# Kernel tuning notes

Hardware: AMD Instinct MI355X
Metric: run time of the kernel (lower is better)

## Reference

```python
import math
import jax, jax.numpy as jnp
import numpy as np

B, E, T, C, D, H, FF, L, NC = 16, 25, 300, 3, 64, 8, 256, 4, 60
HD = D // H
EPS = 1e-5


def _ln(x, g, b):
    mu = x.mean(-1, keepdims=True)
    var = ((x - mu) ** 2).mean(-1, keepdims=True)
    return (x - mu) * jax.lax.rsqrt(var + EPS) * g + b


def _pos_encoding(seq_len, d):
    pos = jnp.arange(seq_len, dtype=jnp.float32)[:, None]
    div = jnp.exp(jnp.arange(0, d, 2, dtype=jnp.float32) * (-math.log(10000.0) / d))
    pe = jnp.zeros((seq_len, d), dtype=jnp.float32)
    pe = pe.at[:, 0::2].set(jnp.sin(pos * div))
    pe = pe.at[:, 1::2].set(jnp.cos(pos * div))
    return pe


def setup_inputs() -> dict:
    key = jax.random.key(0)
    ks = jax.random.split(key, 16)
    tn = lambda k, shape: jax.random.truncated_normal(k, -2.0, 2.0, shape, jnp.float32) * 0.02
    inp = {
        "x": jax.random.normal(ks[0], (B, C, T, E), jnp.float32),
        "embed_w": tn(ks[1], (D, C)), "embed_b": jnp.zeros((D,)),
        "eln_g": jnp.ones((D,)), "eln_b": jnp.zeros((D,)),
        "cls": tn(ks[2], (D,)),
        "qkv_w": tn(ks[3], (L, 3 * D, D)), "qkv_b": jnp.zeros((L, 3 * D)),
        "out_w": tn(ks[4], (L, D, D)), "out_b": jnp.zeros((L, D)),
        "ln1_g": jnp.ones((L, D)), "ln1_b": jnp.zeros((L, D)),
        "ln2_g": jnp.ones((L, D)), "ln2_b": jnp.zeros((L, D)),
        "ff1_w": tn(ks[5], (L, FF, D)), "ff1_b": jnp.zeros((L, FF)),
        "ff2_w": tn(ks[6], (L, D, FF)), "ff2_b": jnp.zeros((L, D)),
        "norm_g": jnp.ones((D,)), "norm_b": jnp.zeros((D,)),
        "h1_w": tn(ks[7], (D, D)), "h1_b": jnp.zeros((D,)),
        "h2_w": tn(ks[8], (NC, D)), "h2_b": jnp.zeros((NC,)),
    }
    return inp


def reference(x, embed_w, embed_b, eln_g, eln_b, cls, qkv_w, qkv_b, out_w, out_b,
              ln1_g, ln1_b, ln2_g, ln2_b, ff1_w, ff1_b, ff2_w, ff2_b,
              norm_g, norm_b, h1_w, h1_b, h2_w, h2_b):
    N, S = B * E, T + 1
    # [B,C,T,E] -> [(B E), T, C]
    h = jnp.transpose(x, (0, 3, 2, 1)).reshape(N, T, C)
    h = _ln(h @ embed_w.T + embed_b, eln_g, eln_b)              # embed + LayerNorm
    h = jnp.concatenate([jnp.broadcast_to(cls, (N, 1, D)), h], axis=1)  # prepend cls
    h = h + _pos_encoding(S, D)
    scale = 1.0 / math.sqrt(HD)
    for l in range(L):  # pre-LN torch TransformerEncoderLayer
        y = _ln(h, ln1_g[l], ln1_b[l])
        qkv = y @ qkv_w[l].T + qkv_b[l]                          # [N,S,3D]
        q, k, v = jnp.split(qkv, 3, axis=-1)
        q = q.reshape(N, S, H, HD).transpose(0, 2, 1, 3)
        k = k.reshape(N, S, H, HD).transpose(0, 2, 1, 3)
        v = v.reshape(N, S, H, HD).transpose(0, 2, 1, 3)
        att = jax.nn.softmax(jnp.einsum("nhqd,nhkd->nhqk", q, k) * scale, axis=-1)
        o = jnp.einsum("nhqk,nhkd->nhqd", att, v).transpose(0, 2, 1, 3).reshape(N, S, D)
        h = h + (o @ out_w[l].T + out_b[l])
        y = _ln(h, ln2_g[l], ln2_b[l])
        h = h + (jax.nn.gelu(y @ ff1_w[l].T + ff1_b[l], approximate=False) @ ff2_w[l].T + ff2_b[l])
    feat = h[:, 0].reshape(B, E, D).mean(axis=1)                 # cls pool, mean over edges
    feat = _ln(feat, norm_g, norm_b)
    feat = jax.nn.gelu(feat @ h1_w.T + h1_b, approximate=False)
    return feat @ h2_w.T + h2_b                                  # [B, num_class]
```

## Files before the change

kernel.cpp:

```cpp
#include <hip/hip_runtime.h>
#include <hip/hip_bf16.h>
#include <math.h>

typedef __hip_bfloat16 bf16;
typedef unsigned short u16;
typedef __attribute__((ext_vector_type(8))) short s8b;
typedef __attribute__((ext_vector_type(4))) short s4h;
typedef __attribute__((ext_vector_type(4))) float f32x4;

#define B_N    16
#define E_N    25
#define T_N    300
#define C_N    3
#define D_N    64
#define H_N    8
#define HD_N   8
#define FF_N   256
#define L_N    4
#define NC_N   60
#define N_SEQ  400
#define S_LEN  301
#define NS_TOT 120400
#define NTILES 7525
#define EPS_F  1e-5f
#define N_IN   24
#define CONV_TOT 568576

#define MFMA16(a, b, c) __builtin_amdgcn_mfma_f32_16x16x32_bf16(a, b, c, 0, 0, 0)

struct ConvArgs { const void* src[N_IN]; };

__device__ __forceinline__ float waveSum(float v) {
#pragma unroll
    for (int off = 32; off > 0; off >>= 1) v += __shfl_xor(v, off, 64);
    return v;
}

__device__ __forceinline__ float gelu_exact(float x) {
    return 0.5f * x * (1.0f + erff(x * 0.70710678118654752f));
}

__device__ __forceinline__ u16 f2b(float x) {
    union { bf16 b; u16 s; } u;
    u.b = __float2bfloat16(x);
    return u.s;
}

__device__ __forceinline__ void split1(float x, short* hi, short* lo) {
    union { bf16 b; short s; } uh, ul;
    uh.b = __float2bfloat16(x);
    ul.b = __float2bfloat16(x - __bfloat162float(uh.b));
    *hi = uh.s; *lo = ul.s;
}

__global__ void convert_kernel(ConvArgs args, float* __restrict__ dst) {
    const int sizes[N_IN] = {360000,192,64,64,64,64,49152,768,16384,256,256,256,
                             256,256,65536,1024,65536,256,64,64,4096,64,3840,60};
    const int offs[N_IN]  = {0,360000,360192,360256,360320,360384,360448,409600,
                             410368,426752,427008,427264,427520,427776,428032,
                             493568,494592,560128,560384,560448,560512,564608,
                             564672,568512};
    int t = blockIdx.x;
    int n = sizes[t];
    bool isbf = (((const unsigned short*)args.src[3])[0] == 0x3F80u);
    float* d = dst + offs[t];
    int start  = threadIdx.x + blockIdx.y * blockDim.x;
    int stride = blockDim.x * gridDim.y;
    if (isbf) {
        const unsigned short* s = (const unsigned short*)args.src[t];
        for (int i = start; i < n; i += stride)
            d[i] = __uint_as_float(((unsigned int)s[i]) << 16);
    } else {
        const float* s = (const float*)args.src[t];
        for (int i = start; i < n; i += stride)
            d[i] = s[i];
    }
}

__global__ void split_kernel(const float* __restrict__ src,
                             short* __restrict__ hi, short* __restrict__ lo,
                             int n) {
    int i = blockIdx.x * 256 + threadIdx.x;
    if (i < n) split1(src[i], &hi[i], &lo[i]);
}

__global__ void embed_kernel(const float* __restrict__ x,
                             const float* __restrict__ ew,
                             const float* __restrict__ ebias,
                             const float* __restrict__ g,
                             const float* __restrict__ bb,
                             const float* __restrict__ cls,
                             float* __restrict__ h) {
    int wave = threadIdx.x >> 6;
    int lane = threadIdx.x & 63;
    int row  = blockIdx.x * 4 + wave;
    if (row >= NS_TOT) return;
    int n = row / S_LEN;
    int s = row - n * S_LEN;
    int d = lane;

    float i2  = (float)(d & ~1);
    float div = expf(i2 * (-0.14391156515f));
    float ang = (float)s * div;
    float pe  = (d & 1) ? cosf(ang) : sinf(ang);

    float val;
    if (s == 0) {
        val = cls[d];
    } else {
        int t = s - 1;
        int bidx = n / E_N;
        int e    = n - bidx * E_N;
        int xb   = ((bidx * C_N + 0) * T_N + t) * E_N + e;
        float x0 = x[xb];
        float x1 = x[xb + T_N * E_N];
        float x2 = x[xb + 2 * T_N * E_N];
        float emb = x0 * ew[d * 3 + 0] + x1 * ew[d * 3 + 1]
                  + x2 * ew[d * 3 + 2] + ebias[d];
        float mu  = waveSum(emb) * (1.0f / 64.0f);
        float c   = emb - mu;
        float var = waveSum(c * c) * (1.0f / 64.0f);
        val = c * rsqrtf(var + EPS_F) * g[d] + bb[d];
    }
    h[row * 64 + d] = val + pe;
}

__global__ void __launch_bounds__(64)
ln_qkv_mfma(const float* __restrict__ h,
            const float* __restrict__ ln_g, const float* __restrict__ ln_b,
            const short* __restrict__ whi,  const float* __restrict__ wb,
            u16* __restrict__ qbuf, u16* __restrict__ kbuf,
            u16* __restrict__ vbuf) {
    __shared__ u16 Yu[2][16 * 72];
    int lane = threadIdx.x;
    int m = lane & 15, quad = lane >> 4;
    int tile0 = blockIdx.x * 2;
    int tile1 = (tile0 + 1 < NTILES) ? tile0 + 1 : tile0;
    bool wr1  = (tile0 + 1 < NTILES);
    int rb[2] = {tile0 * 16, tile1 * 16};

    float4 gv = ((const float4*)ln_g)[m], bv = ((const float4*)ln_b)[m];
    s8b A[2][2];

#pragma unroll
    for (int tt = 0; tt < 2; tt++) {
        const float4* h4 = (const float4*)(h + (size_t)rb[tt] * 64);
#pragma unroll
        for (int t = 0; t < 4; t++) {
            int r = t * 4 + quad;
            float4 v = h4[r * 16 + m];
            float s  = v.x + v.y + v.z + v.w;
            float ss = v.x*v.x + v.y*v.y + v.z*v.z + v.w*v.w;
#pragma unroll
            for (int off = 1; off < 16; off <<= 1) {
                s  += __shfl_xor(s,  off, 64);
                ss += __shfl_xor(ss, off, 64);
            }
            float mu = s * (1.0f / 64.0f);
            float rs = rsqrtf(ss * (1.0f / 64.0f) - mu * mu + EPS_F);
            s4h y;
            y[0] = (short)f2b((v.x - mu) * rs * gv.x + bv.x);
            y[1] = (short)f2b((v.y - mu) * rs * gv.y + bv.y);
            y[2] = (short)f2b((v.z - mu) * rs * gv.z + bv.z);
            y[3] = (short)f2b((v.w - mu) * rs * gv.w + bv.w);
            *(s4h*)&Yu[tt][r * 72 + m * 4] = y;
        }
#pragma unroll
        for (int kt = 0; kt < 2; kt++)
            A[tt][kt] = *(const s8b*)&Yu[tt][m * 72 + kt * 32 + quad * 8];
    }

    int nn[2][4], ssq[2][4];
#pragma unroll
    for (int tt = 0; tt < 2; tt++)
#pragma unroll
        for (int reg = 0; reg < 4; reg++) {
            int row = rb[tt] + quad * 4 + reg;
            nn[tt][reg]  = row / S_LEN;
            ssq[tt][reg] = row - nn[tt][reg] * S_LEN;
        }

    const float scale = 0.35355339059327373f;
    f32x4 zero = {0.f, 0.f, 0.f, 0.f};
#pragma unroll
    for (int nt = 0; nt < 12; nt++) {
        const short* p = whi + (nt * 16 + m) * 64 + quad * 8;
        s8b bh0 = *(const s8b*)p;
        s8b bh1 = *(const s8b*)(p + 32);
        float bias = wb[nt * 16 + m];
        u16* dst = (nt < 4) ? qbuf : (nt < 8) ? kbuf : vbuf;
        float mul = (nt < 4) ? scale : 1.0f;
        int o64  = (nt & 3) * 16 + m;
        int head = o64 >> 3, j = o64 & 7;
#pragma unroll
        for (int tt = 0; tt < 2; tt++) {
            f32x4 c = zero;
            c = MFMA16(A[tt][0], bh0, c);
            c = MFMA16(A[tt][1], bh1, c);
            if (tt == 1 && !wr1) continue;
#pragma unroll
            for (int reg = 0; reg < 4; reg++)
                dst[(((nn[tt][reg] * 8 + head) * S_LEN + ssq[tt][reg]) << 3) + j]
                    = f2b((c[reg] + bias) * mul);
        }
    }
}

__global__ void __launch_bounds__(256)
attn_mfma(u16* __restrict__ qb, const u16* __restrict__ kb,
          const u16* __restrict__ vb) {
    __shared__ u16 Khi[320 * 8];
    __shared__ u16 Vthi[9 * 330];
    __shared__ u16 Pbuf[4][16 * 40];

    int head = blockIdx.x, n = blockIdx.y;
    int tid  = threadIdx.x;
    int wv   = tid >> 6, lane = tid & 63;
    int m    = lane & 15, quad = lane >> 4;
    size_t base = ((size_t)(n * 8 + head)) * S_LEN * 8;

    {
        s8b zero8 = {0,0,0,0,0,0,0,0};
        for (int i = tid; i < 320; i += 256) {
            s8b v = (i < 301) ? *(const s8b*)(kb + base + (size_t)i * 8) : zero8;
            *(s8b*)&Khi[i * 8] = v;
        }
    }
    for (int s = tid; s < 320; s += 256) {
        union { s8b v; u16 e[8]; } row;
        row.v = (s8b){0,0,0,0,0,0,0,0};
        u16 one = 0;
        if (s < 301) {
            row.v = *(const s8b*)(vb + base + (size_t)s * 8);
            one = 0x3F80u;
        }
#pragma unroll
        for (int d = 0; d < 8; d++) Vthi[d * 330 + s] = row.e[d];
        Vthi[8 * 330 + s] = one;
    }
    __syncthreads();

    u16* Pw = &Pbuf[wv][0];

    for (int qt = wv; qt < 19; qt += 4) {
        int qbase = qt * 16;
        s8b Aq = {0,0,0,0,0,0,0,0};
        if (quad == 0) {
            int qr = qbase + m; if (qr > 300) qr = 300;
            Aq = *(const s8b*)(qb + base + (size_t)qr * 8);
        }

        f32x4 oacc = {0.f, 0.f, 0.f, 0.f};
        for (int c = 0; c < 10; c++) {
#pragma unroll
            for (int hh = 0; hh < 2; hh++) {
                int kcol = (2 * c + hh) * 16 + m;
                s8b bh = *(const s8b*)&Khi[kcol * 8];
                f32x4 sc = {0.f, 0.f, 0.f, 0.f};
                sc = MFMA16(Aq, bh, sc);
#pragma unroll
                for (int r = 0; r < 4; r++)
                    Pw[(quad * 4 + r) * 40 + hh * 16 + m] = f2b(__expf(sc[r]));
            }
            s8b Ap = *(const s8b*)&Pw[m * 40 + quad * 8];
            int vrow = (m <= 8) ? m : 8;
            s8b bvh = *(const s8b*)&Vthi[vrow * 330 + c * 32 + quad * 8];
            oacc = MFMA16(Ap, bvh, oacc);
        }

#pragma unroll
        for (int r = 0; r < 4; r++) {
            float l = __shfl(oacc[r], (lane & 48) | 8, 64);
            int qr = qbase + quad * 4 + r;
            if (m < 8 && qr < 301)
                qb[base + (size_t)qr * 8 + m] = f2b(oacc[r] / l);
        }
    }
}

__global__ void __launch_bounds__(64)
outproj_mfma(float* __restrict__ h, const u16* __restrict__ qbuf,
             const short* __restrict__ wohi, const float* __restrict__ wob) {
    __shared__ u16 oLs[2][16 * 72];
    int lane = threadIdx.x;
    int m = lane & 15, quad = lane >> 4;
    int tile0 = blockIdx.x * 2;
    int tile1 = (tile0 + 1 < NTILES) ? tile0 + 1 : tile0;
    bool wr1  = (tile0 + 1 < NTILES);
    int rb[2] = {tile0 * 16, tile1 * 16};

    s8b A[2][2];
#pragma unroll
    for (int tt = 0; tt < 2; tt++) {
        for (int i = lane; i < 1024; i += 64) {
            int r = i >> 6, k = i & 63;
            int row = rb[tt] + r;
            int n = row / S_LEN, s = row - n * S_LEN;
            int head = k >> 3, j = k & 7;
            oLs[tt][r * 72 + k] = qbuf[(((n * 8 + head) * S_LEN + s) << 3) + j];
        }
#pragma unroll
        for (int kt = 0; kt < 2; kt++)
            A[tt][kt] = *(const s8b*)&oLs[tt][m * 72 + kt * 32 + quad * 8];
    }

    f32x4 zero = {0.f, 0.f, 0.f, 0.f};
#pragma unroll
    for (int nt = 0; nt < 4; nt++) {
        const short* p = wohi + (nt * 16 + m) * 64 + quad * 8;
        s8b bh0 = *(const s8b*)p;
        s8b bh1 = *(const s8b*)(p + 32);
        int col = nt * 16 + m;
        float bias = wob[col];
#pragma unroll
        for (int tt = 0; tt < 2; tt++) {
            f32x4 c = zero;
            c = MFMA16(A[tt][0], bh0, c);
            c = MFMA16(A[tt][1], bh1, c);
            if (tt == 1 && !wr1) continue;
#pragma unroll
            for (int reg = 0; reg < 4; reg++) {
                int row = rb[tt] + quad * 4 + reg;
                h[(size_t)row * 64 + col] += c[reg] + bias;
            }
        }
    }
}

__global__ void __launch_bounds__(64)
ln_ff_mfma(float* __restrict__ h,
           const float* __restrict__ g2,  const float* __restrict__ b2,
           const short* __restrict__ w1hi, const float* __restrict__ b1,
           const short* __restrict__ w2hi, const float* __restrict__ b2b) {
    __shared__ u16 Yu[2][16 * 72];
    __shared__ u16 Ts[2][16 * 40];

    int lane = threadIdx.x;
    int m = lane & 15, quad = lane >> 4;
    int tile0 = blockIdx.x * 2;
    int tile1 = (tile0 + 1 < NTILES) ? tile0 + 1 : tile0;
    bool wr1  = (tile0 + 1 < NTILES);
    int rb[2] = {tile0 * 16, tile1 * 16};

    float4 gv = ((const float4*)g2)[m], bv = ((const float4*)b2)[m];
    s8b A1[2][2];

#pragma unroll
    for (int tt = 0; tt < 2; tt++) {
        const float4* h4 = (const float4*)(h + (size_t)rb[tt] * 64);
#pragma unroll
        for (int t = 0; t < 4; t++) {
            int r = t * 4 + quad;
            float4 v = h4[r * 16 + m];
            float s  = v.x + v.y + v.z + v.w;
            float ss = v.x*v.x + v.y*v.y + v.z*v.z + v.w*v.w;
#pragma unroll
            for (int off = 1; off < 16; off <<= 1) {
                s  += __shfl_xor(s,  off, 64);
                ss += __shfl_xor(ss, off, 64);
            }
            float mu = s * (1.0f / 64.0f);
            float rs = rsqrtf(ss * (1.0f / 64.0f) - mu * mu + EPS_F);
            s4h y;
            y[0] = (short)f2b((v.x - mu) * rs * gv.x + bv.x);
            y[1] = (short)f2b((v.y - mu) * rs * gv.y + bv.y);
            y[2] = (short)f2b((v.z - mu) * rs * gv.z + bv.z);
            y[3] = (short)f2b((v.w - mu) * rs * gv.w + bv.w);
            *(s4h*)&Yu[tt][r * 72 + m * 4] = y;
        }
#pragma unroll
        for (int kt = 0; kt < 2; kt++)
            A1[tt][kt] = *(const s8b*)&Yu[tt][m * 72 + kt * 32 + quad * 8];
    }

    f32x4 zero = {0.f, 0.f, 0.f, 0.f};
    f32x4 acc2[2][4] = {{zero, zero, zero, zero}, {zero, zero, zero, zero}};

    for (int kt2 = 0; kt2 < 8; kt2++) {
#pragma unroll
        for (int half = 0; half < 2; half++) {
            int nt = kt2 * 2 + half;
            const short* p = w1hi + (nt * 16 + m) * 64 + quad * 8;
            s8b bh0 = *(const s8b*)p;
            s8b bh1 = *(const s8b*)(p + 32);
            float bias = b1[nt * 16 + m];
#pragma unroll
            for (int tt = 0; tt < 2; tt++) {
                f32x4 c = zero;
                c = MFMA16(A1[tt][0], bh0, c);
                c = MFMA16(A1[tt][1], bh1, c);
#pragma unroll
                for (int reg = 0; reg < 4; reg++)
                    Ts[tt][(quad * 4 + reg) * 40 + half * 16 + m] =
                        f2b(gelu_exact(c[reg] + bias));
            }
        }

        s8b A2[2];
#pragma unroll
        for (int tt = 0; tt < 2; tt++)
            A2[tt] = *(const s8b*)&Ts[tt][m * 40 + quad * 8];
#pragma unroll
        for (int nt2 = 0; nt2 < 4; nt2++) {
            const short* p = w2hi + (nt2 * 16 + m) * 256 + kt2 * 32 + quad * 8;
            s8b bh = *(const s8b*)p;
#pragma unroll
            for (int tt = 0; tt < 2; tt++)
                acc2[tt][nt2] = MFMA16(A2[tt], bh, acc2[tt][nt2]);
        }
    }

#pragma unroll
    for (int tt = 0; tt < 2; tt++) {
        if (tt == 1 && !wr1) break;
#pragma unroll
        for (int nt2 = 0; nt2 < 4; nt2++) {
            int col = nt2 * 16 + m;
            float bias = b2b[col];
#pragma unroll
            for (int reg = 0; reg < 4; reg++) {
                int row = quad * 4 + reg;
                float* hp = h + (size_t)(rb[tt] + row) * 64 + col;
                *hp += acc2[tt][nt2][reg] + bias;
            }
        }
    }
}

__global__ void head_kernel(const float* __restrict__ h,
                            const float* __restrict__ ng,
                            const float* __restrict__ nb,
                            const float* __restrict__ w1,
                            const float* __restrict__ b1,
                            const float* __restrict__ w2,
                            const float* __restrict__ b2,
                            float* __restrict__ out) {
    __shared__ float feat[64];
    __shared__ float g1[64];
    int b = blockIdx.x, d = threadIdx.x;

    float s = 0.f;
    for (int e = 0; e < E_N; e++)
        s += h[(size_t)((b * E_N + e) * S_LEN) * 64 + d];
    s *= (1.0f / 25.0f);

    float mu  = waveSum(s) * (1.0f / 64.0f);
    float c   = s - mu;
    float var = waveSum(c * c) * (1.0f / 64.0f);
    feat[d] = c * rsqrtf(var + EPS_F) * ng[d] + nb[d];
    __syncthreads();

    float a = b1[d];
    for (int k = 0; k < 64; k++) a += feat[k] * w1[d * 64 + k];
    g1[d] = gelu_exact(a);
    __syncthreads();

    if (d < NC_N) {
        float a2 = b2[d];
        for (int k = 0; k < 64; k++) a2 += g1[k] * w2[d * 64 + k];
        out[b * NC_N + d] = a2;
    }
}

extern "C" void kernel_launch(void* const* d_in, const int* in_sizes, int n_in,
                              void* d_out, int out_size, void* d_ws, size_t ws_size,
                              hipStream_t stream) {
    ConvArgs ca;
    for (int i = 0; i < N_IN; i++) ca.src[i] = d_in[i];

    float* F = (float*)d_ws;
    const int offs[N_IN] = {0,360000,360192,360256,360320,360384,360448,409600,
                            410368,426752,427008,427264,427520,427776,428032,
                            493568,494592,560128,560384,560448,560512,564608,
                            564672,568512};
    const float* x       = F + offs[0];
    const float* embed_w = F + offs[1];
    const float* embed_b = F + offs[2];
    const float* eln_g   = F + offs[3];
    const float* eln_b   = F + offs[4];
    const float* cls     = F + offs[5];
    const float* qkv_w   = F + offs[6];
    const float* qkv_b   = F + offs[7];
    const float* out_w   = F + offs[8];
    const float* out_b   = F + offs[9];
    const float* ln1_g   = F + offs[10];
    const float* ln1_b   = F + offs[11];
    const float* ln2_g   = F + offs[12];
    const float* ln2_b   = F + offs[13];
    const float* ff1_w   = F + offs[14];
    const float* ff1_b   = F + offs[15];
    const float* ff2_w   = F + offs[16];
    const float* ff2_b   = F + offs[17];
    const float* norm_g  = F + offs[18];
    const float* norm_b  = F + offs[19];
    const float* h1_w    = F + offs[20];
    const float* h1_b    = F + offs[21];
    const float* h2_w    = F + offs[22];
    const float* h2_b    = F + offs[23];

    float* h   = F + CONV_TOT;
    u16* qbuf = (u16*)(h + (size_t)NS_TOT * 64);
    u16* kbuf = qbuf + (size_t)NS_TOT * 64;
    u16* vbuf = kbuf + (size_t)NS_TOT * 64;
    short* qwhi = (short*)(vbuf + (size_t)NS_TOT * 64);
    short* qwlo = qwhi + 49152;
    short* w1hi = qwlo + 49152;
    short* w1lo = w1hi + 65536;
    short* w2hi = w1lo + 65536;
    short* w2lo = w2hi + 65536;
    short* wohi = w2lo + 65536;
    short* wolo = wohi + 16384;

    convert_kernel<<<dim3(N_IN, 8), 256, 0, stream>>>(ca, F);
    split_kernel<<<192, 256, 0, stream>>>(qkv_w, qwhi, qwlo, 49152);
    split_kernel<<<256, 256, 0, stream>>>(ff1_w, w1hi, w1lo, 65536);
    split_kernel<<<256, 256, 0, stream>>>(ff2_w, w2hi, w2lo, 65536);
    split_kernel<<<64, 256, 0, stream>>>(out_w, wohi, wolo, 16384);

    embed_kernel<<<NS_TOT / 4, 256, 0, stream>>>(x, embed_w, embed_b,
                                                 eln_g, eln_b, cls, h);

    for (int l = 0; l < L_N; l++) {
        ln_qkv_mfma<<<(NTILES + 1) / 2, 64, 0, stream>>>(
            h, ln1_g + l * 64, ln1_b + l * 64,
            qwhi + l * 12288, qkv_b + l * 192,
            qbuf, kbuf, vbuf);
        attn_mfma<<<dim3(H_N, N_SEQ), 256, 0, stream>>>(qbuf, kbuf, vbuf);
        outproj_mfma<<<(NTILES + 1) / 2, 64, 0, stream>>>(
            h, qbuf, wohi + l * 4096, out_b + l * 64);
        ln_ff_mfma<<<(NTILES + 1) / 2, 64, 0, stream>>>(
            h, ln2_g + l * 64, ln2_b + l * 64,
            w1hi + l * 16384, ff1_b + l * 256,
            w2hi + l * 16384, ff2_b + l * 64);
    }

    head_kernel<<<B_N, 64, 0, stream>>>(h, norm_g, norm_b,
                                        h1_w, h1_b, h2_w, h2_b,
                                        (float*)d_out);
}
```

Before: 745.0 us.

## Fuse out-projection with LN2+FFN kernel and use truncating bf16 conversion

Merges the attention out-projection kernel with the LayerNorm+FFN kernel. The residual sum now stays in registers and LN2 is computed directly from the MFMA accumulators, which removes one launch per layer and a full read-modify-write round trip of h through global memory. It also replaces round-to-nearest float-to-bf16 conversion with plain truncation (top 16 bits) in the QKV, attention, and FFN paths. Truncation biases rounding and slightly lowers accuracy, and the fused kernel holds more live registers.

```diff
diff --git a/kernel.cpp b/kernel.cpp
--- a/kernel.cpp
+++ b/kernel.cpp
@@ -44,6 +44,10 @@
     union { bf16 b; u16 s; } u;
     u.b = __float2bfloat16(x);
     return u.s;
+}
+
+__device__ __forceinline__ u16 f2b_t(float x) {
+    return (u16)(__float_as_uint(x) >> 16);
 }
 
 __device__ __forceinline__ void split1(float x, short* hi, short* lo) {
@@ -159,10 +163,10 @@
             float mu = s * (1.0f / 64.0f);
             float rs = rsqrtf(ss * (1.0f / 64.0f) - mu * mu + EPS_F);
             s4h y;
-            y[0] = (short)f2b((v.x - mu) * rs * gv.x + bv.x);
-            y[1] = (short)f2b((v.y - mu) * rs * gv.y + bv.y);
-            y[2] = (short)f2b((v.z - mu) * rs * gv.z + bv.z);
-            y[3] = (short)f2b((v.w - mu) * rs * gv.w + bv.w);
+            y[0] = (short)f2b_t((v.x - mu) * rs * gv.x + bv.x);
+            y[1] = (short)f2b_t((v.y - mu) * rs * gv.y + bv.y);
+            y[2] = (short)f2b_t((v.z - mu) * rs * gv.z + bv.z);
+            y[3] = (short)f2b_t((v.w - mu) * rs * gv.w + bv.w);
             *(s4h*)&Yu[tt][r * 72 + m * 4] = y;
         }
 #pragma unroll
@@ -201,7 +205,7 @@
 #pragma unroll
             for (int reg = 0; reg < 4; reg++)
                 dst[(((nn[tt][reg] * 8 + head) * S_LEN + ssq[tt][reg]) << 3) + j]
-                    = f2b((c[reg] + bias) * mul);
+                    = f2b_t((c[reg] + bias) * mul);
         }
     }
 }
@@ -260,7 +264,7 @@
                 sc = MFMA16(Aq, bh, sc);
 #pragma unroll
                 for (int r = 0; r < 4; r++)
-                    Pw[(quad * 4 + r) * 40 + hh * 16 + m] = f2b(__expf(sc[r]));
+                    Pw[(quad * 4 + r) * 40 + hh * 16 + m] = f2b_t(__expf(sc[r]));
             }
             s8b Ap = *(const s8b*)&Pw[m * 40 + quad * 8];
             int vrow = (m <= 8) ? m : 8;
@@ -273,15 +277,20 @@
             float l = __shfl(oacc[r], (lane & 48) | 8, 64);
             int qr = qbase + quad * 4 + r;
             if (m < 8 && qr < 301)
-                qb[base + (size_t)qr * 8 + m] = f2b(oacc[r] / l);
+                qb[base + (size_t)qr * 8 + m] = f2b_t(oacc[r] / l);
         }
     }
 }
 
 __global__ void __launch_bounds__(64)
-outproj_mfma(float* __restrict__ h, const u16* __restrict__ qbuf,
-             const short* __restrict__ wohi, const float* __restrict__ wob) {
+out_ff_mfma(float* __restrict__ h, const u16* __restrict__ qbuf,
+            const short* __restrict__ wohi, const float* __restrict__ wob,
+            const float* __restrict__ g2,  const float* __restrict__ b2,
+            const short* __restrict__ w1hi, const float* __restrict__ b1,
+            const short* __restrict__ w2hi, const float* __restrict__ b2b) {
     __shared__ u16 oLs[2][16 * 72];
+    __shared__ u16 Ts[2][16 * 40];
+
     int lane = threadIdx.x;
     int m = lane & 15, quad = lane >> 4;
     int tile0 = blockIdx.x * 2;
@@ -289,7 +298,7 @@
     bool wr1  = (tile0 + 1 < NTILES);
     int rb[2] = {tile0 * 16, tile1 * 16};
 
-    s8b A[2][2];
+    s8b AO[2][2];
 #pragma unroll
     for (int tt = 0; tt < 2; tt++) {
         for (int i = lane; i < 1024; i += 64) {
@@ -301,10 +310,11 @@
         }
 #pragma unroll
         for (int kt = 0; kt < 2; kt++)
-            A[tt][kt] = *(const s8b*)&oLs[tt][m * 72 + kt * 32 + quad * 8];
+            AO[tt][kt] = *(const s8b*)&oLs[tt][m * 72 + kt * 32 + quad * 8];
     }
 
     f32x4 zero = {0.f, 0.f, 0.f, 0.f};
+    float hnew[2][4][4];
 #pragma unroll
     for (int nt = 0; nt < 4; nt++) {
         const short* p = wohi + (nt * 16 + m) * 64 + quad * 8;
@@ -315,45 +325,27 @@
 #pragma unroll
         for (int tt = 0; tt < 2; tt++) {
             f32x4 c = zero;
-            c = MFMA16(A[tt][0], bh0, c);
-            c = MFMA16(A[tt][1], bh1, c);
-            if (tt == 1 && !wr1) continue;
+            c = MFMA16(AO[tt][0], bh0, c);
+            c = MFMA16(AO[tt][1], bh1, c);
 #pragma unroll
             for (int reg = 0; reg < 4; reg++) {
                 int row = rb[tt] + quad * 4 + reg;
-                h[(size_t)row * 64 + col] += c[reg] + bias;
-            }
-        }
-    }
-}
-
-__global__ void __launch_bounds__(64)
-ln_ff_mfma(float* __restrict__ h,
-           const float* __restrict__ g2,  const float* __restrict__ b2,
-           const short* __restrict__ w1hi, const float* __restrict__ b1,
-           const short* __restrict__ w2hi, const float* __restrict__ b2b) {
-    __shared__ u16 Yu[2][16 * 72];
-    __shared__ u16 Ts[2][16 * 40];
-
-    int lane = threadIdx.x;
-    int m = lane & 15, quad = lane >> 4;
-    int tile0 = blockIdx.x * 2;
-    int tile1 = (tile0 + 1 < NTILES) ? tile0 + 1 : tile0;
-    bool wr1  = (tile0 + 1 < NTILES);
-    int rb[2] = {tile0 * 16, tile1 * 16};
-
-    float4 gv = ((const float4*)g2)[m], bv = ((const float4*)b2)[m];
+                hnew[tt][nt][reg] = h[(size_t)row * 64 + col] + c[reg] + bias;
+            }
+        }
+    }
+
     s8b A1[2][2];
-
 #pragma unroll
     for (int tt = 0; tt < 2; tt++) {
-        const float4* h4 = (const float4*)(h + (size_t)rb[tt] * 64);
-#pragma unroll
-        for (int t = 0; t < 4; t++) {
-            int r = t * 4 + quad;
-            float4 v = h4[r * 16 + m];
-            float s  = v.x + v.y + v.z + v.w;
-            float ss = v.x*v.x + v.y*v.y + v.z*v.z + v.w*v.w;
+#pragma unroll
+        for (int reg = 0; reg < 4; reg++) {
+            float s  = hnew[tt][0][reg] + hnew[tt][1][reg]
+                     + hnew[tt][2][reg] + hnew[tt][3][reg];
+            float ss = hnew[tt][0][reg]*hnew[tt][0][reg]
+                     + hnew[tt][1][reg]*hnew[tt][1][reg]
+                     + hnew[tt][2][reg]*hnew[tt][2][reg]
+                     + hnew[tt][3][reg]*hnew[tt][3][reg];
 #pragma unroll
             for (int off = 1; off < 16; off <<= 1) {
                 s  += __shfl_xor(s,  off, 64);
@@ -361,21 +353,19 @@
             }
             float mu = s * (1.0f / 64.0f);
             float rs = rsqrtf(ss * (1.0f / 64.0f) - mu * mu + EPS_F);
-            s4h y;
-            y[0] = (short)f2b((v.x - mu) * rs * gv.x + bv.x);
-            y[1] = (short)f2b((v.y - mu) * rs * gv.y + bv.y);
-            y[2] = (short)f2b((v.z - mu) * rs * gv.z + bv.z);
-            y[3] = (short)f2b((v.w - mu) * rs * gv.w + bv.w);
-            *(s4h*)&Yu[tt][r * 72 + m * 4] = y;
+#pragma unroll
+            for (int nt = 0; nt < 4; nt++) {
+                int col = nt * 16 + m;
+                oLs[tt][(quad * 4 + reg) * 72 + col] =
+                    f2b_t((hnew[tt][nt][reg] - mu) * rs * g2[col] + b2[col]);
+            }
         }
 #pragma unroll
         for (int kt = 0; kt < 2; kt++)
-            A1[tt][kt] = *(const s8b*)&Yu[tt][m * 72 + kt * 32 + quad * 8];
-    }
-
-    f32x4 zero = {0.f, 0.f, 0.f, 0.f};
+            A1[tt][kt] = *(const s8b*)&oLs[tt][m * 72 + kt * 32 + quad * 8];
+    }
+
     f32x4 acc2[2][4] = {{zero, zero, zero, zero}, {zero, zero, zero, zero}};
-
     for (int kt2 = 0; kt2 < 8; kt2++) {
 #pragma unroll
         for (int half = 0; half < 2; half++) {
@@ -392,7 +382,7 @@
 #pragma unroll
                 for (int reg = 0; reg < 4; reg++)
                     Ts[tt][(quad * 4 + reg) * 40 + half * 16 + m] =
-                        f2b(gelu_exact(c[reg] + bias));
+                        f2b_t(gelu_exact(c[reg] + bias));
             }
         }
 
@@ -419,9 +409,9 @@
             float bias = b2b[col];
 #pragma unroll
             for (int reg = 0; reg < 4; reg++) {
-                int row = quad * 4 + reg;
-                float* hp = h + (size_t)(rb[tt] + row) * 64 + col;
-                *hp += acc2[tt][nt2][reg] + bias;
+                int row = rb[tt] + quad * 4 + reg;
+                h[(size_t)row * 64 + col] =
+                    hnew[tt][nt2][reg] + acc2[tt][nt2][reg] + bias;
             }
         }
     }
@@ -526,10 +516,10 @@
             qwhi + l * 12288, qkv_b + l * 192,
             qbuf, kbuf, vbuf);
         attn_mfma<<<dim3(H_N, N_SEQ), 256, 0, stream>>>(qbuf, kbuf, vbuf);
-        outproj_mfma<<<(NTILES + 1) / 2, 64, 0, stream>>>(
-            h, qbuf, wohi + l * 4096, out_b + l * 64);
-        ln_ff_mfma<<<(NTILES + 1) / 2, 64, 0, stream>>>(
-            h, ln2_g + l * 64, ln2_b + l * 64,
+        out_ff_mfma<<<(NTILES + 1) / 2, 64, 0, stream>>>(
+            h, qbuf,
+            wohi + l * 4096, out_b + l * 64,
+            ln2_g + l * 64, ln2_b + l * 64,
             w1hi + l * 16384, ff1_b + l * 256,
             w2hi + l * 16384, ff2_b + l * 64);
     }
```

Measured after the change: 741.3 us (median of 2 runs). About the same (-0.5%).
